# Performance work log

Hardware: AMD Instinct MI355X
Metric: run time of the kernel (lower is better)

## Reference

```python
import jax, jax.numpy as jnp
import numpy as np

WS, EXP, FW, HEADS = 7, 3, 7, 6
DIM = 192
HD = DIM // HEADS
SCALE = HD ** -0.5
POOL_K, POOL_PAD = 7, 3  # focal level k=0: kernel = 2*(FW//2) + 2**0 + (2**0 - 1) = 7, stride 1, pad 3
WA = WS * WS  # 49 tokens per window


def _rel_index():
    # identical formula for in-window bias and pooled-window bias (k_window = FW + 2**0 - 1 = 7 = WS)
    c = np.stack(np.meshgrid(np.arange(WS), np.arange(WS), indexing='ij')).reshape(2, -1)
    rel = (c[:, :, None] - c[:, None, :]).transpose(1, 2, 0).copy()
    rel[..., 0] += WS - 1
    rel[..., 1] += WS - 1
    rel[..., 0] *= 2 * WS - 1
    return rel.sum(-1)  # (49, 49) int indices into 169-entry tables


def _valid_rolled():
    m = np.ones((4, WS, WS), dtype=np.float32)
    m[0, :-EXP, :-EXP] = 0  # tl
    m[1, :-EXP, EXP:] = 0   # tr
    m[2, EXP:, :-EXP] = 0   # bl
    m[3, EXP:, EXP:] = 0    # br
    return np.nonzero(m.reshape(-1))[0]  # (132,)

REL_IDX = _rel_index()
VALID_ROLLED = _valid_rolled()


def _win_part(t):
    # (B,H,W,C) -> (B*nWin, WA, HEADS, HD)
    B, H, W, C = t.shape
    t = t.reshape(B, H // WS, WS, W // WS, WS, C).transpose(0, 1, 3, 2, 4, 5)
    return t.reshape(-1, WA, HEADS, HD)


def _unfold(t):
    # torch.nn.Unfold(kernel=7, stride=1, pad=3) on (B,h,w,C) -> (B*h*w, K*K, C)
    B, h, w, C = t.shape
    tp = jnp.pad(t, ((0, 0), (POOL_PAD, POOL_PAD), (POOL_PAD, POOL_PAD), (0, 0)))
    ii = np.arange(h)[:, None] + np.arange(POOL_K)[None, :]
    jj = np.arange(w)[:, None] + np.arange(POOL_K)[None, :]
    p = tp[:, ii][:, :, :, jj]            # (B, h, K, w, K, C)
    p = p.transpose(0, 1, 3, 2, 4, 5)     # (B, h, w, K, K, C)
    return p.reshape(B * h * w, POOL_K * POOL_K, C)


def setup_inputs() -> dict:
    key = jax.random.key(0)
    ks = jax.random.split(key, 9)
    B, H, W = 8, 112, 112
    nWh, nWw = H // WS, W // WS
    return {
        'x': jax.random.normal(ks[0], (B, H, W, DIM), jnp.float32),
        'x_pooled': jax.random.normal(ks[1], (B, nWh, nWw, DIM), jnp.float32),
        'qkv_w': jax.random.normal(ks[2], (3 * DIM, DIM), jnp.float32) * 0.02,
        'qkv_b': jax.random.normal(ks[3], (3 * DIM,), jnp.float32) * 0.02,
        'proj_w': jax.random.normal(ks[4], (DIM, DIM), jnp.float32) * 0.02,
        'proj_b': jax.random.normal(ks[5], (DIM,), jnp.float32) * 0.02,
        'rpb_table': jax.random.normal(ks[6], ((2 * WS - 1) ** 2, HEADS), jnp.float32) * 0.02,
        'rpb_neighbors': jax.random.normal(ks[7], (1, HEADS, WA, len(VALID_ROLLED)), jnp.float32) * 0.02,
        'rpb_windows': jax.random.normal(ks[8], (HEADS, (2 * WS - 1) ** 2), jnp.float32) * 0.02,
    }


def reference(x, x_pooled, qkv_w, qkv_b, proj_w, proj_b, rpb_table, rpb_neighbors, rpb_windows):
    B, H, W, C = x.shape
    # qkv on fine features
    qkv = x @ qkv_w.T + qkv_b                    # (B,H,W,3C)
    q, k, v = jnp.split(qkv, 3, axis=-1)
    qw = _win_part(q).transpose(0, 2, 1, 3)      # (BnW, heads, 49, hd)
    kw = _win_part(k).transpose(0, 2, 1, 3)
    vw = _win_part(v).transpose(0, 2, 1, 3)

    # rolled neighbor keys/values (tl, tr, bl, br), gather valid ring indices
    shifts = [(-EXP, -EXP), (-EXP, EXP), (EXP, -EXP), (EXP, EXP)]
    k_roll = jnp.concatenate([_win_part(jnp.roll(k, s, axis=(1, 2))) for s in shifts], axis=1)
    v_roll = jnp.concatenate([_win_part(jnp.roll(v, s, axis=(1, 2))) for s in shifts], axis=1)
    k_roll = k_roll.transpose(0, 2, 1, 3)[:, :, VALID_ROLLED]   # (BnW, heads, 132, hd)
    v_roll = v_roll.transpose(0, 2, 1, 3)[:, :, VALID_ROLLED]
    k_rolled = jnp.concatenate([kw, k_roll], axis=2)            # (BnW, heads, 181, hd)
    v_rolled = jnp.concatenate([vw, v_roll], axis=2)
    wa_rolled = k_rolled.shape[2]

    # focal level-0 pooled keys/values via unfold on the pooled map
    _, nWh, nWw, _ = x_pooled.shape
    qkv_p = x_pooled @ qkv_w.T + qkv_b
    _, kp, vp = jnp.split(qkv_p, 3, axis=-1)
    k_pool = _unfold(kp).reshape(-1, POOL_K * POOL_K, HEADS, HD).transpose(0, 2, 1, 3)  # (BnW, heads, 49, hd)
    v_pool = _unfold(vp).reshape(-1, POOL_K * POOL_K, HEADS, HD).transpose(0, 2, 1, 3)
    # validity mask from unfolding an all-ones map (zero padding -> -100)
    um = _unfold(jnp.ones((1, nWh, nWw, 1), x.dtype))[..., 0]   # (nWin, 49)
    pool_mask = jnp.where(um == 0, jnp.asarray(-100.0, x.dtype), jnp.asarray(0.0, x.dtype))

    k_all = jnp.concatenate([k_rolled, k_pool], axis=2)          # (BnW, heads, 230, hd)
    v_all = jnp.concatenate([v_rolled, v_pool], axis=2)

    attn = jnp.einsum('bhqd,bhkd->bhqk', qw * SCALE, k_all)      # (BnW, heads, 49, 230)

    # relative position biases, concatenated along the key axis
    bias_win = rpb_table[REL_IDX.reshape(-1)].reshape(WA, WA, HEADS).transpose(2, 0, 1)     # (heads,49,49)
    bias_pool = rpb_windows[:, REL_IDX.reshape(-1)].reshape(HEADS, WA, WA)                  # (heads,49,49)
    bias = jnp.concatenate([bias_win, rpb_neighbors[0], bias_pool], axis=-1)                # (heads,49,230)
    attn = attn + bias[None]
    # boundary mask on the pooled slice, tiled per batch
    mask_b = jnp.tile(pool_mask, (B, 1))[:, None, None, :]       # (BnW,1,1,49)
    attn = attn.at[..., wa_rolled:].add(mask_b)

    attn = jax.nn.softmax(attn, axis=-1)
    out = jnp.einsum('bhqk,bhkd->bqhd', attn, v_all).reshape(-1, WA, C)
    return out @ proj_w.T + proj_b                               # (B*nWin, 49, C)
```

## Files before the change

kernel.cpp:

```cpp
#include <hip/hip_runtime.h>
#include <stdint.h>


#define DIM 192
#define HEADS 6
#define HD 32
#define WA 49
#define NKEY 230
#define SSTR 272
#define VSTR 264
#define SCALE_F 0.17677669529663687f
#define NFINE 100352
#define POOLBASE (NFINE * DIM)

typedef __attribute__((ext_vector_type(8))) short bf16x8;
typedef __attribute__((ext_vector_type(4))) float f32x4;

__device__ __forceinline__ short f2bf(float f) {
  union { float f; uint32_t u; } v; v.f = f;
  uint32_t u = v.u;
  return (short)((u + 0x7FFFu + ((u >> 16) & 1u)) >> 16);
}

__device__ __forceinline__ float bf2f(short s) {
  union { uint32_t u; float f; } v;
  v.u = ((uint32_t)(uint16_t)s) << 16;
  return v.f;
}

__global__ __launch_bounds__(256) void k_setup(
    const float* __restrict__ qkv_w, const float* __restrict__ proj_w,
    const float* __restrict__ rpb_table, const float* __restrict__ rpb_nb,
    const float* __restrict__ rpb_win,
    short* __restrict__ w1, short* __restrict__ w1s, short* __restrict__ w2s,
    int* __restrict__ t_idx, short* __restrict__ bias_bf) {
  __shared__ int2 ring_s[132];
  if (threadIdx.x < 132) {
    int e = threadIdx.x;
    int cnt = 0, fdr = 0, fdc = 0;
    for (int idx = 0; idx < 196; ++idx) {
      int s = idx / 49, rc = idx % 49, r = rc / 7, c = rc % 7;
      bool valid;
      if (s == 0)      valid = (r >= 4) || (c >= 4);
      else if (s == 1) valid = (r >= 4) || (c < 3);
      else if (s == 2) valid = (r < 3)  || (c >= 4);
      else             valid = (r < 3)  || (c < 3);
      if (valid) {
        if (cnt == e) { fdr = r + ((s < 2) ? 3 : -3); fdc = c + (((s & 1) == 0) ? 3 : -3); }
        ++cnt;
      }
    }
    ring_s[e] = make_int2(fdr, fdc);
  }
  __syncthreads();

  const int tid = blockIdx.x * blockDim.x + threadIdx.x;
  const int nth = gridDim.x * blockDim.x;
  for (int i = tid; i < 576 * DIM; i += nth) {
    float fv = qkv_w[i];
    w1[i] = f2bf(fv);
    int r = i / DIM, c = i % DIM;
    int t = r >> 5, ntl = (r >> 4) & 1, lr = r & 15;
    int ks = c >> 5, quad = (c >> 3) & 3, e = c & 7;
    w1s[t * 6144 + (((ntl * 6 + ks) * 4 + quad) * 16 + lr) * 8 + e] = f2bf(fv);
  }
  for (int i = tid; i < DIM * DIM; i += nth) {
    int r = i / DIM, c = i % DIM;
    int t = r >> 5, ntl = (r >> 4) & 1, lr = r & 15;
    int ks = c >> 5, quad = (c >> 3) & 3, e = c & 7;
    w2s[t * 6144 + (((ntl * 6 + ks) * 4 + quad) * 16 + lr) * 8 + e] = f2bf(proj_w[i]);
  }
  for (int i = tid; i < 2048 * NKEY; i += nth) {
    int win = i / NKEY, kk = i - win * NKEY;
    int b = win >> 8, wr = (win >> 4) & 15, wc = win & 15;
    int off;
    if (kk < 49) {
      int ii = wr * 7 + kk / 7, jj = wc * 7 + kk % 7;
      off = ((b * 112 + ii) * 112 + jj) * DIM;
    } else if (kk < 181) {
      int2 rr = ring_s[kk - 49];
      int ii = wr * 7 + rr.x; if (ii < 0) ii += 112; if (ii >= 112) ii -= 112;
      int jj = wc * 7 + rr.y; if (jj < 0) jj += 112; if (jj >= 112) jj -= 112;
      off = ((b * 112 + ii) * 112 + jj) * DIM;
    } else {
      int p = kk - 181;
      int ii = wr - 3 + p / 7, jj = wc - 3 + p % 7;
      off = (ii >= 0 && ii < 16 && jj >= 0 && jj < 16)
              ? (POOLBASE + ((b * 16 + ii) * 16 + jj) * DIM) : -1;
    }
    t_idx[(win << 8) + kk] = off;
  }
  for (int i = tid; i < HEADS * 15 * 1024; i += nth) {
    int row = i & 63, l16v = (i >> 6) & 15;
    int rem = i >> 10, nt = rem % 15, h = rem / 15;
    int kk = nt * 16 + l16v;
    float bv = 0.f;
    if (kk >= NKEY) {
      bv = -1e30f;
    } else if (row < WA) {
      if (kk < 49) {
        int ar = row / 7, ac = row % 7, br = kk / 7, bc = kk % 7;
        bv = rpb_table[((ar - br + 6) * 13 + (ac - bc + 6)) * HEADS + h];
      } else if (kk < 181) {
        bv = rpb_nb[((size_t)h * WA + row) * 132 + (kk - 49)];
      } else {
        int p = kk - 181;
        int ar = row / 7, ac = row % 7, br = p / 7, bc = p % 7;
        bv = rpb_win[h * 169 + (ar - br + 6) * 13 + (ac - bc + 6)];
      }
    }
    bias_bf[i] = f2bf(bv);
  }
}

__global__ __launch_bounds__(256, 4) void k_qkv_main(
    const float* __restrict__ x, const short* __restrict__ w1s, const float* __restrict__ qkv_b,
    short* __restrict__ qw, short* __restrict__ kn, short* __restrict__ vn) {
  __shared__ __align__(16) short wbuf[2][6144];
  const int tid = threadIdx.x;
  const int wave = tid >> 6, lane = tid & 63, quad = lane >> 4, l16 = lane & 15;
  const int mbase = blockIdx.x * 128;

  bf16x8 afr[2][6];
#pragma unroll
  for (int mt = 0; mt < 2; ++mt) {
    const float* xrow = x + (size_t)(mbase + wave * 32 + mt * 16 + l16) * DIM + quad * 8;
#pragma unroll
    for (int ks = 0; ks < 6; ++ks) {
      float4 f0 = *(const float4*)(xrow + ks * 32);
      float4 f1 = *(const float4*)(xrow + ks * 32 + 4);
      bf16x8 a;
      a[0] = f2bf(f0.x); a[1] = f2bf(f0.y); a[2] = f2bf(f0.z); a[3] = f2bf(f0.w);
      a[4] = f2bf(f1.x); a[5] = f2bf(f1.y); a[6] = f2bf(f1.z); a[7] = f2bf(f1.w);
      afr[mt][ks] = a;
    }
  }
  uint32_t q_base[2][4], kv_base[2][4];
#pragma unroll
  for (int mt = 0; mt < 2; ++mt)
#pragma unroll
    for (int rg = 0; rg < 4; ++rg) {
      int m = mbase + wave * 32 + mt * 16 + quad * 4 + rg;
      int bb = m / 12544, rem = m % 12544;
      int i = rem / 112, j = rem % 112;
      int wr = i / 7, rr = i % 7, wc = j / 7, cc = j % 7;
      int winid = (bb * 16 + wr) * 16 + wc;
      q_base[mt][rg]  = ((uint32_t)winid * WA + (rr * 7 + cc)) * DIM;
      kv_base[mt][rg] = (uint32_t)m * DIM;
    }

  int4 st[3];
  {
    const int4* src = (const int4*)w1s + tid;
#pragma unroll
    for (int it = 0; it < 3; ++it) st[it] = src[it * 256];
  }
  for (int t = 0; t < 18; ++t) {
    short* buf = wbuf[t & 1];
#pragma unroll
    for (int it = 0; it < 3; ++it) ((int4*)buf)[tid + it * 256] = st[it];
    __syncthreads();
    if (t < 17) {
      const int4* src = (const int4*)(w1s + (t + 1) * 6144) + tid;
#pragma unroll
      for (int it = 0; it < 3; ++it) st[it] = src[it * 256];
    }
#pragma unroll
    for (int ntl = 0; ntl < 2; ++ntl) {
      const int n = t * 32 + ntl * 16 + l16;
      bf16x8 bfr[6];
#pragma unroll
      for (int ks = 0; ks < 6; ++ks)
        bfr[ks] = *(const bf16x8*)&buf[(((ntl * 6 + ks) * 4 + quad) * 16 + l16) * 8];
      const float bias = qkv_b[n];
#pragma unroll
      for (int mt = 0; mt < 2; ++mt) {
        f32x4 acc = {0.f, 0.f, 0.f, 0.f};
#pragma unroll
        for (int ks = 0; ks < 6; ++ks)
          acc = __builtin_amdgcn_mfma_f32_16x16x32_bf16(afr[mt][ks], bfr[ks], acc, 0, 0, 0);
#pragma unroll
        for (int rg = 0; rg < 4; ++rg) {
          float vo = acc[rg] + bias;
          if (t < 6)       qw[q_base[mt][rg] + n]           = f2bf(vo * SCALE_F);
          else if (t < 12) kn[kv_base[mt][rg] + (n - 192)]  = f2bf(vo);
          else             vn[kv_base[mt][rg] + (n - 384)]  = f2bf(vo);
        }
      }
    }
  }
}

__global__ __launch_bounds__(256) void k_qkv_pool(
    const float* __restrict__ xp, const short* __restrict__ w1, const float* __restrict__ qkv_b,
    short* __restrict__ kp, short* __restrict__ vp) {
  const int tid = threadIdx.x;
  const int wave = tid >> 6, lane = tid & 63, quad = lane >> 4, l16 = lane & 15;
  const int mbase = (blockIdx.x * 4 + wave) * 16;

  bf16x8 afr[6];
  {
    const float* xrow = xp + (size_t)(mbase + l16) * DIM + quad * 8;
#pragma unroll
    for (int ks = 0; ks < 6; ++ks) {
      float4 f0 = *(const float4*)(xrow + ks * 32);
      float4 f1 = *(const float4*)(xrow + ks * 32 + 4);
      bf16x8 a;
      a[0] = f2bf(f0.x); a[1] = f2bf(f0.y); a[2] = f2bf(f0.z); a[3] = f2bf(f0.w);
      a[4] = f2bf(f1.x); a[5] = f2bf(f1.y); a[6] = f2bf(f1.z); a[7] = f2bf(f1.w);
      afr[ks] = a;
    }
  }
  for (int nt = 12; nt < 36; ++nt) {
    const int n = nt * 16 + l16;
    const short* wrow = w1 + (size_t)n * DIM + quad * 8;
    f32x4 acc = {0.f, 0.f, 0.f, 0.f};
#pragma unroll
    for (int ks = 0; ks < 6; ++ks)
      acc = __builtin_amdgcn_mfma_f32_16x16x32_bf16(afr[ks], *(const bf16x8*)(wrow + ks * 32), acc, 0, 0, 0);
    const float bias = qkv_b[n];
#pragma unroll
    for (int rg = 0; rg < 4; ++rg) {
      int m = mbase + quad * 4 + rg;
      float vo = acc[rg] + bias;
      if (nt < 24) kp[(size_t)m * DIM + (n - 192)] = f2bf(vo);
      else         vp[(size_t)m * DIM + (n - 384)] = f2bf(vo);
    }
  }
}

__global__ __launch_bounds__(256, 3) void k_attn(
    const short* __restrict__ qw, const short* __restrict__ kall, const short* __restrict__ vall,
    const short* __restrict__ bias_bf, const int* __restrict__ t_idx,
    short* __restrict__ ao) {
  __shared__ __align__(16) char smem[52736];
  short* vT_l  = (short*)smem;
  short* k_l   = (short*)(smem + 16896);
  short* q_l   = (short*)(smem + 16896 + 19200);
  short* S_l   = (short*)(smem + 16896);
  float* pmask = (float*)(smem + 51712);

  const int tid = threadIdx.x;
  const int bid = ((int)blockIdx.x & 7) * 1536 + ((int)blockIdx.x >> 3);
  const int win = bid / HEADS;
  const int h   = bid - win * HEADS;
  const int wr  = (win >> 4) & 15;
  const int wc  = win & 15;
  const int wave = tid >> 6, lane = tid & 63, quad = lane >> 4, l16 = lane & 15;

  {
    int* kli = (int*)k_l;
    for (int i = tid; i < 200; i += 256) kli[4600 + i] = 0;
    int* qli = (int*)q_l;
    for (int i = tid; i < 300; i += 256) qli[980 + i] = 0;
    if (tid < 128) {
      int ch = tid >> 2, j = tid & 3;
      *(int4*)&vT_l[ch * VSTR + ((224 + j * 8) ^ (((ch >> 3) & 3) << 4))] = make_int4(0, 0, 0, 0);
    }
    {
      float pm = 0.f;
      if (tid >= 181 && tid < NKEY) {
        int p = tid - 181;
        int pi = wr - 3 + p / 7, pj = wc - 3 + p % 7;
        if (pi < 0 || pi >= 16 || pj < 0 || pj >= 16) pm = -100.f;
      }
      pmask[tid] = pm;
    }
  }
  __syncthreads();

  if (tid < 196) {
    int r = tid >> 2, part = tid & 3;
    *(int4*)&q_l[r * 40 + part * 8] =
        *(const int4*)(qw + ((size_t)win * WA + r) * DIM + h * HD + part * 8);
  }
  {
    const int part = tid & 3;
    const int choff = h * HD + part * 8;
    const int* tix = t_idx + (win << 8);
#pragma unroll
    for (int it = 0; it < 4; ++it) {
      int kk = it * 64 + (tid >> 2);
      if (kk < NKEY) {
        int off = tix[kk];
        int4 kvv = make_int4(0, 0, 0, 0), vvv = make_int4(0, 0, 0, 0);
        if (off >= 0) {
          kvv = *(const int4*)(kall + off + choff);
          vvv = *(const int4*)(vall + off + choff);
        }
        *(int4*)&k_l[kk * 40 + part * 8] = kvv;
        const short* vs = (const short*)&vvv;
        const int kkx = kk ^ (part << 4);
#pragma unroll
        for (int e = 0; e < 8; ++e) vT_l[(part * 8 + e) * VSTR + kkx] = vs[e];
      }
    }
  }
  __syncthreads();

  f32x4 acc[15];
  {
    bf16x8 qfr = *(const bf16x8*)&q_l[(wave * 16 + l16) * 40 + quad * 8];
#pragma unroll
    for (int nt = 0; nt < 15; ++nt) {
      bf16x8 kfr = *(const bf16x8*)&k_l[(nt * 16 + l16) * 40 + quad * 8];
      f32x4 z = {0.f, 0.f, 0.f, 0.f};
      acc[nt] = __builtin_amdgcn_mfma_f32_16x16x32_bf16(qfr, kfr, z, 0, 0, 0);
    }
  }
  const int rowb = wave * 16 + quad * 4;
  {
    const short* bb = bias_bf + ((size_t)(h * 15 * 16 + l16)) * 64 + rowb;
#pragma unroll
    for (int nt = 0; nt < 15; ++nt) {
      int2 braw = *(const int2*)(bb + nt * 1024);
      const short* bs = (const short*)&braw;
      const float pm = pmask[nt * 16 + l16];
#pragma unroll
      for (int rg = 0; rg < 4; ++rg)
        acc[nt][rg] = acc[nt][rg] + bf2f(bs[rg]) + pm;
    }
  }
  float m4[4] = {-1e30f, -1e30f, -1e30f, -1e30f};
#pragma unroll
  for (int nt = 0; nt < 15; ++nt)
#pragma unroll
    for (int rg = 0; rg < 4; ++rg) m4[rg] = fmaxf(m4[rg], acc[nt][rg]);
#pragma unroll
  for (int msk = 1; msk <= 8; msk <<= 1)
#pragma unroll
    for (int rg = 0; rg < 4; ++rg) m4[rg] = fmaxf(m4[rg], __shfl_xor(m4[rg], msk));
  float s4[4] = {0.f, 0.f, 0.f, 0.f};
#pragma unroll
  for (int nt = 0; nt < 15; ++nt)
#pragma unroll
    for (int rg = 0; rg < 4; ++rg) {
      float e = __expf(acc[nt][rg] - m4[rg]);
      acc[nt][rg] = e; s4[rg] += e;
    }
#pragma unroll
  for (int msk = 1; msk <= 8; msk <<= 1)
#pragma unroll
    for (int rg = 0; rg < 4; ++rg) s4[rg] += __shfl_xor(s4[rg], msk);
  float inv4[4];
#pragma unroll
  for (int rg = 0; rg < 4; ++rg) inv4[rg] = 1.f / s4[rg];
#pragma unroll
  for (int nt = 0; nt < 15; ++nt)
#pragma unroll
    for (int rg = 0; rg < 4; ++rg) acc[nt][rg] *= inv4[rg];

  __syncthreads();

#pragma unroll
  for (int nt = 0; nt < 15; ++nt)
#pragma unroll
    for (int rg = 0; rg < 4; ++rg)
      S_l[(rowb + rg) * SSTR + ((nt * 16 + l16) ^ (quad << 4))] = f2bf(acc[nt][rg]);
  {
    int rr = tid >> 2, c0 = 240 + (tid & 3) * 4;
    *(int2*)&S_l[rr * SSTR + (c0 ^ (((rr >> 2) & 3) << 4))] = make_int2(0, 0);
  }
  __syncthreads();

  const int fsr = (l16 >> 2) << 4;
#pragma unroll
  for (int nt2 = 0; nt2 < 2; ++nt2) {
    f32x4 acc2 = {0.f, 0.f, 0.f, 0.f};
    const int fvr = (((nt2 * 16 + l16) >> 3) & 3) << 4;
#pragma unroll
    for (int k0 = 0; k0 < 8; ++k0) {
      bf16x8 pfr = *(const bf16x8*)&S_l[(wave * 16 + l16) * SSTR + ((k0 * 32 + quad * 8) ^ fsr)];
      bf16x8 vfr = *(const bf16x8*)&vT_l[(nt2 * 16 + l16) * VSTR + ((k0 * 32 + quad * 8) ^ fvr)];
      acc2 = __builtin_amdgcn_mfma_f32_16x16x32_bf16(pfr, vfr, acc2, 0, 0, 0);
    }
#pragma unroll
    for (int rg = 0; rg < 4; ++rg) {
      int row = rowb + rg;
      if (row < WA)
        ao[((size_t)win * WA + row) * DIM + h * HD + nt2 * 16 + l16] = f2bf(acc2[rg]);
    }
  }
}

__global__ __launch_bounds__(256, 4) void k_proj(
    const short* __restrict__ ao, const short* __restrict__ w2s, const float* __restrict__ pb,
    float* __restrict__ out) {
  __shared__ __align__(16) short wbuf[2][6144];
  const int tid = threadIdx.x;
  const int wave = tid >> 6, lane = tid & 63, quad = lane >> 4, l16 = lane & 15;
  const int mbase = blockIdx.x * 128;

  bf16x8 afr[2][6];
#pragma unroll
  for (int mt = 0; mt < 2; ++mt) {
    const short* arow = ao + (size_t)(mbase + wave * 32 + mt * 16 + l16) * DIM + quad * 8;
#pragma unroll
    for (int ks = 0; ks < 6; ++ks) afr[mt][ks] = *(const bf16x8*)(arow + ks * 32);
  }
  int4 st[3];
  {
    const int4* src = (const int4*)w2s + tid;
#pragma unroll
    for (int it = 0; it < 3; ++it) st[it] = src[it * 256];
  }
  for (int t = 0; t < 6; ++t) {
    short* buf = wbuf[t & 1];
#pragma unroll
    for (int it = 0; it < 3; ++it) ((int4*)buf)[tid + it * 256] = st[it];
    __syncthreads();
    if (t < 5) {
      const int4* src = (const int4*)(w2s + (t + 1) * 6144) + tid;
#pragma unroll
      for (int it = 0; it < 3; ++it) st[it] = src[it * 256];
    }
#pragma unroll
    for (int ntl = 0; ntl < 2; ++ntl) {
      const int n = t * 32 + ntl * 16 + l16;
      bf16x8 bfr[6];
#pragma unroll
      for (int ks = 0; ks < 6; ++ks)
        bfr[ks] = *(const bf16x8*)&buf[(((ntl * 6 + ks) * 4 + quad) * 16 + l16) * 8];
      const float bias = pb[n];
#pragma unroll
      for (int mt = 0; mt < 2; ++mt) {
        f32x4 acc = {0.f, 0.f, 0.f, 0.f};
#pragma unroll
        for (int ks = 0; ks < 6; ++ks)
          acc = __builtin_amdgcn_mfma_f32_16x16x32_bf16(afr[mt][ks], bfr[ks], acc, 0, 0, 0);
#pragma unroll
        for (int rg = 0; rg < 4; ++rg)
          out[(size_t)(mbase + wave * 32 + mt * 16 + quad * 4 + rg) * DIM + n] = acc[rg] + bias;
      }
    }
  }
}

extern "C" void kernel_launch(void* const* d_in, const int* in_sizes, int n_in,
                              void* d_out, int out_size, void* d_ws, size_t ws_size,
                              hipStream_t stream) {
  (void)in_sizes; (void)n_in; (void)out_size; (void)ws_size;
  const float* x         = (const float*)d_in[0];
  const float* xp        = (const float*)d_in[1];
  const float* qkv_w     = (const float*)d_in[2];
  const float* qkv_b     = (const float*)d_in[3];
  const float* proj_w    = (const float*)d_in[4];
  const float* proj_b    = (const float*)d_in[5];
  const float* rpb_table = (const float*)d_in[6];
  const float* rpb_nb    = (const float*)d_in[7];
  const float* rpb_win   = (const float*)d_in[8];

  char* ws = (char*)d_ws;
  size_t off = 0;
  auto alloc = [&](size_t bytes) -> void* {
    void* p = ws + off; off = (off + bytes + 255) & ~(size_t)255; return p;
  };
  short* w1       = (short*)alloc((size_t)576 * DIM * 2);
  short* w1s      = (short*)alloc((size_t)576 * DIM * 2);
  short* w2s      = (short*)alloc((size_t)DIM * DIM * 2);
  short* bias_bf  = (short*)alloc((size_t)HEADS * 15 * 1024 * 2);
  int*   t_idx    = (int*)  alloc((size_t)2048 * 256 * 4);
  short* qw       = (short*)alloc((size_t)2048 * WA * DIM * 2);
  short* kall     = (short*)alloc((size_t)(NFINE + 2048) * DIM * 2);
  short* vall     = (short*)alloc((size_t)(NFINE + 2048) * DIM * 2);
  short* ao       = (short*)alloc((size_t)2048 * WA * DIM * 2);

  k_setup<<<dim3(64), dim3(256), 0, stream>>>(qkv_w, proj_w, rpb_table, rpb_nb, rpb_win,
                                              w1, w1s, w2s, t_idx, bias_bf);
  k_qkv_main<<<dim3(784), dim3(256), 0, stream>>>(x, w1s, qkv_b, qw, kall, vall);
  k_qkv_pool<<<dim3(32), dim3(256), 0, stream>>>(xp, w1, qkv_b,
                                                 kall + (size_t)POOLBASE, vall + (size_t)POOLBASE);
  k_attn<<<dim3(12288), dim3(256), 0, stream>>>(qw, kall, vall, bias_bf, t_idx, ao);
  k_proj<<<dim3(784), dim3(256), 0, stream>>>(ao, w2s, proj_b, (float*)d_out);
}
```

Baseline: 511.1 us.

## Shrink attention LDS to raise occupancy; split P·V into two halves, defer normalization

```diff
diff --git a/kernel.cpp b/kernel.cpp
--- a/kernel.cpp
+++ b/kernel.cpp
@@ -7,8 +7,8 @@
 #define HD 32
 #define WA 49
 #define NKEY 230
-#define SSTR 272
 #define VSTR 264
+#define SSTR2 136
 #define SCALE_F 0.17677669529663687f
 #define NFINE 100352
 #define POOLBASE (NFINE * DIM)
@@ -26,6 +26,12 @@
   union { uint32_t u; float f; } v;
   v.u = ((uint32_t)(uint16_t)s) << 16;
   return v.f;
+}
+
+__device__ __forceinline__ uint32_t cvtpk(float lo, float hi) {
+  uint32_t r;
+  asm("v_cvt_pk_bf16_f32 %0, %1, %2" : "=v"(r) : "v"(lo), "v"(hi));
+  return r;
 }
 
 __global__ __launch_bounds__(256) void k_setup(
@@ -173,18 +179,36 @@
       for (int ks = 0; ks < 6; ++ks)
         bfr[ks] = *(const bf16x8*)&buf[(((ntl * 6 + ks) * 4 + quad) * 16 + l16) * 8];
       const float bias = qkv_b[n];
+      f32x4 ac[2];
 #pragma unroll
       for (int mt = 0; mt < 2; ++mt) {
-        f32x4 acc = {0.f, 0.f, 0.f, 0.f};
+        f32x4 a = {0.f, 0.f, 0.f, 0.f};
 #pragma unroll
         for (int ks = 0; ks < 6; ++ks)
-          acc = __builtin_amdgcn_mfma_f32_16x16x32_bf16(afr[mt][ks], bfr[ks], acc, 0, 0, 0);
+          a = __builtin_amdgcn_mfma_f32_16x16x32_bf16(afr[mt][ks], bfr[ks], a, 0, 0, 0);
+        ac[mt] = a;
+      }
+      if (t < 6) {
+        const float bq = bias * SCALE_F;
 #pragma unroll
         for (int rg = 0; rg < 4; ++rg) {
-          float vo = acc[rg] + bias;
-          if (t < 6)       qw[q_base[mt][rg] + n]           = f2bf(vo * SCALE_F);
-          else if (t < 12) kn[kv_base[mt][rg] + (n - 192)]  = f2bf(vo);
-          else             vn[kv_base[mt][rg] + (n - 384)]  = f2bf(vo);
+          uint32_t r = cvtpk(fmaf(ac[0][rg], SCALE_F, bq), fmaf(ac[1][rg], SCALE_F, bq));
+          qw[q_base[0][rg] + n] = (short)r;
+          qw[q_base[1][rg] + n] = (short)(r >> 16);
+        }
+      } else if (t < 12) {
+#pragma unroll
+        for (int rg = 0; rg < 4; ++rg) {
+          uint32_t r = cvtpk(ac[0][rg] + bias, ac[1][rg] + bias);
+          kn[kv_base[0][rg] + (n - 192)] = (short)r;
+          kn[kv_base[1][rg] + (n - 192)] = (short)(r >> 16);
+        }
+      } else {
+#pragma unroll
+        for (int rg = 0; rg < 4; ++rg) {
+          uint32_t r = cvtpk(ac[0][rg] + bias, ac[1][rg] + bias);
+          vn[kv_base[0][rg] + (n - 384)] = (short)r;
+          vn[kv_base[1][rg] + (n - 384)] = (short)(r >> 16);
         }
       }
     }
@@ -229,16 +253,15 @@
   }
 }
 
-__global__ __launch_bounds__(256, 3) void k_attn(
+__global__ __launch_bounds__(256, 4) void k_attn(
     const short* __restrict__ qw, const short* __restrict__ kall, const short* __restrict__ vall,
     const short* __restrict__ bias_bf, const int* __restrict__ t_idx,
     short* __restrict__ ao) {
-  __shared__ __align__(16) char smem[52736];
+  __shared__ __align__(16) char smem[37120];
   short* vT_l  = (short*)smem;
   short* k_l   = (short*)(smem + 16896);
-  short* q_l   = (short*)(smem + 16896 + 19200);
   short* S_l   = (short*)(smem + 16896);
-  float* pmask = (float*)(smem + 51712);
+  float* pmask = (float*)(smem + 36096);
 
   const int tid = threadIdx.x;
   const int bid = ((int)blockIdx.x & 7) * 1536 + ((int)blockIdx.x >> 3);
@@ -251,29 +274,26 @@
   {
     int* kli = (int*)k_l;
     for (int i = tid; i < 200; i += 256) kli[4600 + i] = 0;
-    int* qli = (int*)q_l;
-    for (int i = tid; i < 300; i += 256) qli[980 + i] = 0;
     if (tid < 128) {
       int ch = tid >> 2, j = tid & 3;
       *(int4*)&vT_l[ch * VSTR + ((224 + j * 8) ^ (((ch >> 3) & 3) << 4))] = make_int4(0, 0, 0, 0);
     }
-    {
-      float pm = 0.f;
-      if (tid >= 181 && tid < NKEY) {
-        int p = tid - 181;
-        int pi = wr - 3 + p / 7, pj = wc - 3 + p % 7;
-        if (pi < 0 || pi >= 16 || pj < 0 || pj >= 16) pm = -100.f;
-      }
-      pmask[tid] = pm;
-    }
-  }
-  __syncthreads();
-
-  if (tid < 196) {
-    int r = tid >> 2, part = tid & 3;
-    *(int4*)&q_l[r * 40 + part * 8] =
-        *(const int4*)(qw + ((size_t)win * WA + r) * DIM + h * HD + part * 8);
-  }
+    float pm = 0.f;
+    if (tid >= 181 && tid < NKEY) {
+      int p = tid - 181;
+      int pi = wr - 3 + p / 7, pj = wc - 3 + p % 7;
+      if (pi < 0 || pi >= 16 || pj < 0 || pj >= 16) pm = -100.f;
+    }
+    pmask[tid] = pm;
+  }
+  bf16x8 qfr = {0, 0, 0, 0, 0, 0, 0, 0};
+  {
+    const int qrow = wave * 16 + l16;
+    if (qrow < WA)
+      qfr = *(const bf16x8*)(qw + ((size_t)win * WA + qrow) * DIM + h * HD + quad * 8);
+  }
+  __syncthreads();
+
   {
     const int part = tid & 3;
     const int choff = h * HD + part * 8;
@@ -299,14 +319,11 @@
   __syncthreads();
 
   f32x4 acc[15];
-  {
-    bf16x8 qfr = *(const bf16x8*)&q_l[(wave * 16 + l16) * 40 + quad * 8];
-#pragma unroll
-    for (int nt = 0; nt < 15; ++nt) {
-      bf16x8 kfr = *(const bf16x8*)&k_l[(nt * 16 + l16) * 40 + quad * 8];
-      f32x4 z = {0.f, 0.f, 0.f, 0.f};
-      acc[nt] = __builtin_amdgcn_mfma_f32_16x16x32_bf16(qfr, kfr, z, 0, 0, 0);
-    }
+#pragma unroll
+  for (int nt = 0; nt < 15; ++nt) {
+    bf16x8 kfr = *(const bf16x8*)&k_l[(nt * 16 + l16) * 40 + quad * 8];
+    f32x4 z = {0.f, 0.f, 0.f, 0.f};
+    acc[nt] = __builtin_amdgcn_mfma_f32_16x16x32_bf16(qfr, kfr, z, 0, 0, 0);
   }
   const int rowb = wave * 16 + quad * 4;
   {
@@ -345,40 +362,70 @@
   float inv4[4];
 #pragma unroll
   for (int rg = 0; rg < 4; ++rg) inv4[rg] = 1.f / s4[rg];
-#pragma unroll
-  for (int nt = 0; nt < 15; ++nt)
-#pragma unroll
-    for (int rg = 0; rg < 4; ++rg) acc[nt][rg] *= inv4[rg];
-
-  __syncthreads();
-
-#pragma unroll
-  for (int nt = 0; nt < 15; ++nt)
-#pragma unroll
-    for (int rg = 0; rg < 4; ++rg)
-      S_l[(rowb + rg) * SSTR + ((nt * 16 + l16) ^ (quad << 4))] = f2bf(acc[nt][rg]);
-  {
-    int rr = tid >> 2, c0 = 240 + (tid & 3) * 4;
-    *(int2*)&S_l[rr * SSTR + (c0 ^ (((rr >> 2) & 3) << 4))] = make_int2(0, 0);
-  }
-  __syncthreads();
-
-  const int fsr = (l16 >> 2) << 4;
+
+  __syncthreads();
+
+  const int swS = ((quad >> 1) & 1) << 4;
+#pragma unroll
+  for (int rg = 0; rg < 4; ++rg) {
+    const int base = (rowb + rg) * SSTR2;
+#pragma unroll
+    for (int p = 0; p < 4; ++p) {
+      uint32_t r = cvtpk(acc[2 * p][rg], acc[2 * p + 1][rg]);
+      S_l[base + ((p * 32 + l16) ^ swS)]      = (short)r;
+      S_l[base + ((p * 32 + 16 + l16) ^ swS)] = (short)(r >> 16);
+    }
+  }
+  __syncthreads();
+
+  const int swR = ((l16 >> 3) & 1) << 4;
+  f32x4 acc2[2] = {{0.f, 0.f, 0.f, 0.f}, {0.f, 0.f, 0.f, 0.f}};
 #pragma unroll
   for (int nt2 = 0; nt2 < 2; ++nt2) {
-    f32x4 acc2 = {0.f, 0.f, 0.f, 0.f};
     const int fvr = (((nt2 * 16 + l16) >> 3) & 3) << 4;
 #pragma unroll
-    for (int k0 = 0; k0 < 8; ++k0) {
-      bf16x8 pfr = *(const bf16x8*)&S_l[(wave * 16 + l16) * SSTR + ((k0 * 32 + quad * 8) ^ fsr)];
+    for (int k0 = 0; k0 < 4; ++k0) {
+      bf16x8 pfr = *(const bf16x8*)&S_l[(wave * 16 + l16) * SSTR2 + ((k0 * 32 + quad * 8) ^ swR)];
       bf16x8 vfr = *(const bf16x8*)&vT_l[(nt2 * 16 + l16) * VSTR + ((k0 * 32 + quad * 8) ^ fvr)];
-      acc2 = __builtin_amdgcn_mfma_f32_16x16x32_bf16(pfr, vfr, acc2, 0, 0, 0);
-    }
-#pragma unroll
-    for (int rg = 0; rg < 4; ++rg) {
-      int row = rowb + rg;
-      if (row < WA)
-        ao[((size_t)win * WA + row) * DIM + h * HD + nt2 * 16 + l16] = f2bf(acc2[rg]);
+      acc2[nt2] = __builtin_amdgcn_mfma_f32_16x16x32_bf16(pfr, vfr, acc2[nt2], 0, 0, 0);
+    }
+  }
+  __syncthreads();
+
+#pragma unroll
+  for (int rg = 0; rg < 4; ++rg) {
+    const int base = (rowb + rg) * SSTR2;
+#pragma unroll
+    for (int p = 0; p < 3; ++p) {
+      uint32_t r = cvtpk(acc[8 + 2 * p][rg], acc[9 + 2 * p][rg]);
+      S_l[base + ((p * 32 + l16) ^ swS)]      = (short)r;
+      S_l[base + ((p * 32 + 16 + l16) ^ swS)] = (short)(r >> 16);
+    }
+    uint32_t r = cvtpk(acc[14][rg], 0.f);
+    S_l[base + ((96 + l16) ^ swS)]  = (short)r;
+    S_l[base + ((112 + l16) ^ swS)] = (short)(r >> 16);
+  }
+  __syncthreads();
+
+#pragma unroll
+  for (int nt2 = 0; nt2 < 2; ++nt2) {
+    const int fvr = (((nt2 * 16 + l16) >> 3) & 3) << 4;
+#pragma unroll
+    for (int k0 = 0; k0 < 4; ++k0) {
+      bf16x8 pfr = *(const bf16x8*)&S_l[(wave * 16 + l16) * SSTR2 + ((k0 * 32 + quad * 8) ^ swR)];
+      bf16x8 vfr = *(const bf16x8*)&vT_l[(nt2 * 16 + l16) * VSTR + ((128 + k0 * 32 + quad * 8) ^ fvr)];
+      acc2[nt2] = __builtin_amdgcn_mfma_f32_16x16x32_bf16(pfr, vfr, acc2[nt2], 0, 0, 0);
+    }
+  }
+
+#pragma unroll
+  for (int rg = 0; rg < 4; ++rg) {
+    const int row = rowb + rg;
+    if (row < WA) {
+      uint32_t r = cvtpk(acc2[0][rg] * inv4[rg], acc2[1][rg] * inv4[rg]);
+      short* dst = ao + ((size_t)win * WA + row) * DIM + h * HD + l16;
+      dst[0]  = (short)r;
+      dst[16] = (short)(r >> 16);
     }
   }
 }
```

Measured after the change: 474.7 us. 7.1% less time.
